# Kernel optimization log

Hardware: AMD Instinct MI355X
Metric: run time of the kernel (lower is better)

The kernel has to match this reference:

```python
import jax, jax.numpy as jnp
import numpy as np


def _gcn_conv(x, W, b, src, dst, num_nodes):
    # PyG GCNConv: h = x @ W; symmetric normalization with self-loops; scatter-add; + bias
    h = x @ W
    deg = jax.ops.segment_sum(jnp.ones_like(dst, dtype=h.dtype), dst, num_segments=num_nodes)
    dinv = jnp.where(deg > 0, jax.lax.rsqrt(deg), 0.0)
    norm = dinv[src] * dinv[dst]                         # [E]
    msgs = h[src] * norm[:, None]                        # [E, H] gather + scale
    out = jax.ops.segment_sum(msgs, dst, num_segments=num_nodes)
    return out + b


def setup_inputs() -> dict:
    key = jax.random.key(0)
    ks = jax.random.split(key, 10)
    N, E = 500000, 1000000
    IN, H, SIG = 3, 64, 24
    x = jax.random.uniform(ks[0], (N, IN), dtype=jnp.float32)
    edge_index = jax.random.randint(ks[1], (2, E), 0, N, dtype=jnp.int64)
    batch = jnp.zeros((N,), dtype=jnp.int64)
    def glorot(k, shape):
        lim = np.sqrt(6.0 / (shape[0] + shape[1]))
        return jax.random.uniform(k, shape, dtype=jnp.float32, minval=-lim, maxval=lim)
    return {
        "x": x,
        "edge_index": edge_index,
        "batch": batch,
        "W1": glorot(ks[2], (IN, H)), "b1": jnp.zeros((H,), jnp.float32),
        "W2": glorot(ks[3], (H, H)),  "b2": jnp.zeros((H,), jnp.float32),
        "W3": glorot(ks[4], (H, H)),  "b3": jnp.zeros((H,), jnp.float32),
        "Wfc": glorot(ks[5], (H, SIG)), "bfc": jnp.zeros((SIG,), jnp.float32),
    }


def reference(x, edge_index, batch, W1, b1, W2, b2, W3, b3, Wfc, bfc):
    N = x.shape[0]
    NUM_GRAPHS = 1  # batch is all zeros (single graph)
    # add self-loops once (GCNConv adds them per layer; identical edge set each layer)
    loop = jnp.arange(N, dtype=edge_index.dtype)
    src = jnp.concatenate([edge_index[0], loop])
    dst = jnp.concatenate([edge_index[1], loop])

    h = jax.nn.relu(_gcn_conv(x, W1, b1, src, dst, N))
    h = jax.nn.relu(_gcn_conv(h, W2, b2, src, dst, N))
    h = jax.nn.relu(_gcn_conv(h, W3, b3, src, dst, N))

    # global mean pool per graph
    sums = jax.ops.segment_sum(h, batch, num_segments=NUM_GRAPHS)          # [G, H]
    counts = jax.ops.segment_sum(jnp.ones((N,), h.dtype), batch, num_segments=NUM_GRAPHS)
    sig = sums / jnp.maximum(counts, 1.0)[:, None]

    return jnp.tanh(sig @ Wfc + bfc)  # [G, 24]
```

## Files before the change

### kernel.cpp

```cpp
#include <hip/hip_runtime.h>
#include <hip/hip_bf16.h>
#include <hip/hip_fp16.h>


#define ALIGN256(x) (((x) + 255) & ~(size_t)255)
#define NBUCK_MAX 512

typedef _Float16 half8 __attribute__((ext_vector_type(8)));
typedef _Float16 half4 __attribute__((ext_vector_type(4)));
typedef float f32x4 __attribute__((ext_vector_type(4)));
typedef int i32x4 __attribute__((ext_vector_type(4)));

__device__ __forceinline__ void dec16(i32x4 r, half8& a, half8& b) {
    i32x4 u, v;
    u.x = (int)(((unsigned)r.x << 8) & 0xFF00FF00u);
    u.y = (int)(((unsigned)r.x)      & 0xFF00FF00u);
    u.z = (int)(((unsigned)r.y << 8) & 0xFF00FF00u);
    u.w = (int)(((unsigned)r.y)      & 0xFF00FF00u);
    v.x = (int)(((unsigned)r.z << 8) & 0xFF00FF00u);
    v.y = (int)(((unsigned)r.z)      & 0xFF00FF00u);
    v.z = (int)(((unsigned)r.w << 8) & 0xFF00FF00u);
    v.w = (int)(((unsigned)r.w)      & 0xFF00FF00u);
    a = *(half8*)&u; b = *(half8*)&v;
}

__device__ __forceinline__ unsigned char enc8(float x) {
    unsigned short hb = __half_as_ushort(__float2half(x));
    return (unsigned char)((hb + 0x80u) >> 8);
}

__global__ __launch_bounds__(256) void hist_kernel(const int* __restrict__ ei, int E, int CE, int SH,
                                                   int* __restrict__ cnt_mat,
                                                   float* __restrict__ pool,
                                                   unsigned char* __restrict__ h8a,
                                                   unsigned char* __restrict__ h8b, int N) {
    __shared__ int h[NBUCK_MAX];
    const int t = threadIdx.x, blk = blockIdx.x;
    if (blk == 0) {
        if (t < 64) pool[t] = 0.f;
        if (t < 16) {
            ((int*)(h8a + (size_t)N * 64))[t] = 0;
            ((int*)(h8b + (size_t)N * 64))[t] = 0;
        }
    }
    for (int i = t; i < NBUCK_MAX; i += 256) h[i] = 0;
    __syncthreads();
    const int e0 = blk * CE, e1 = min(E, e0 + CE);
    for (int e = e0 + t; e < e1; e += 256)
        atomicAdd(&h[ei[E + e] >> SH], 1);
    __syncthreads();
    for (int i = t; i < NBUCK_MAX; i += 256) cnt_mat[blk * NBUCK_MAX + i] = h[i];
}

__global__ __launch_bounds__(64) void colscan_kernel(const int* __restrict__ cnt_mat,
                                                     int* __restrict__ base_mat,
                                                     int* __restrict__ tot, int nblk) {
    __shared__ int ls[64];
    const int j = blockIdx.x;
    const int t = threadIdx.x;
    const int PER = (nblk + 63) >> 6;
    const int b0 = t * PER, b1 = min(nblk, b0 + PER);
    int s = 0;
    for (int b = b0; b < b1; ++b) s += cnt_mat[b * NBUCK_MAX + j];
    ls[t] = s;
    __syncthreads();
    if (t == 0) {
        int run = 0;
        for (int k = 0; k < 64; ++k) { int v = ls[k]; ls[k] = run; run += v; }
        tot[j] = run;
    }
    __syncthreads();
    int run = ls[t];
    for (int b = b0; b < b1; ++b) {
        int v = cnt_mat[b * NBUCK_MAX + j];
        base_mat[b * NBUCK_MAX + j] = run;
        run += v;
    }
}

__global__ __launch_bounds__(256) void totscan_kernel(const int* __restrict__ tot,
                                                      int* __restrict__ startb, int NBK, int E) {
    __shared__ int ls[256];
    const int t = threadIdx.x;
    const int PER = (NBK + 255) >> 8;
    const int j0 = t * PER, j1 = min(NBK, j0 + PER);
    int s = 0;
    for (int j = j0; j < j1; ++j) s += tot[j];
    ls[t] = s;
    __syncthreads();
    if (t == 0) {
        int run = 0;
        for (int k = 0; k < 256; ++k) { int v = ls[k]; ls[k] = run; run += v; }
        startb[NBK] = E;
    }
    __syncthreads();
    int run = ls[t];
    for (int j = j0; j < j1; ++j) { startb[j] = run; run += tot[j]; }
}

__global__ __launch_bounds__(256) void scatter_kernel(const int* __restrict__ ei, int E, int CE, int SH,
                                                      const int* __restrict__ base_mat,
                                                      const int* __restrict__ start,
                                                      unsigned* __restrict__ bkt) {
    __shared__ int sbuf[4096];
    __shared__ unsigned short sb[4096];
    __shared__ int lh[NBUCK_MAX];
    __shared__ int lbase[NBUCK_MAX];
    __shared__ int cur[NBUCK_MAX];
    __shared__ int ls[256];
    const int t = threadIdx.x, blk = blockIdx.x;
    for (int i = t; i < NBUCK_MAX; i += 256) { lh[i] = 0; cur[i] = 0; }
    __syncthreads();
    const int e0 = blk * CE, e1 = min(E, e0 + CE);
    for (int e = e0 + t; e < e1; e += 256)
        atomicAdd(&lh[ei[E + e] >> SH], 1);
    __syncthreads();
    int a0 = lh[2 * t], a1 = lh[2 * t + 1];
    ls[t] = a0 + a1;
    __syncthreads();
    if (t == 0) {
        int run = 0;
        for (int k = 0; k < 256; ++k) { int v = ls[k]; ls[k] = run; run += v; }
    }
    __syncthreads();
    lbase[2 * t]     = ls[t];
    lbase[2 * t + 1] = ls[t] + a0;
    __syncthreads();
    const unsigned lowm = (1u << SH) - 1u;
    for (int e = e0 + t; e < e1; e += 256) {
        int s = ei[e], d = ei[E + e];
        int b = d >> SH;
        int r = atomicAdd(&cur[b], 1);
        int slot = lbase[b] + r;
        sbuf[slot] = (int)((((unsigned)d & lowm) << 21) | (unsigned)s);
        sb[slot] = (unsigned short)b;
    }
    __syncthreads();
    const int n = e1 - e0;
    for (int i = t; i < n; i += 256) {
        int b = sb[i];
        int dest = start[b] + base_mat[blk * NBUCK_MAX + b] + (i - lbase[b]);
        bkt[dest] = (unsigned)sbuf[i];
    }
}

__global__ __launch_bounds__(256) void build_kernel(const unsigned* __restrict__ bkt,
                                                    const int* __restrict__ start,
                                                    int SH, int nrows, int N,
                                                    const float* __restrict__ x,
                                                    int* __restrict__ ell, int* __restrict__ sec,
                                                    half4* __restrict__ xs) {
    __shared__ __align__(16) int loc[2048][8];
    const int t = threadIdx.x, j = blockIdx.x;
    const int R = 1 << SH;
    int4 z = make_int4(0, 0, 0, 0);
    for (int i = t; i < R * 2; i += 256) ((int4*)loc)[i] = z;
    __syncthreads();
    const int s0 = start[j], s1 = start[j + 1];
    for (int e = s0 + t; e < s1; e += 256) {
        unsigned p = bkt[e];
        int dl = (int)(p >> 21);
        int src = (int)(p & 0x1FFFFFu);
        int k = atomicAdd(&loc[dl][0], 1);
        if (k < 7) loc[dl][1 + k] = src;
        else if (k < 15) {
            int grow = (j << SH) + dl;
            sec[(size_t)grow * 8 + (k - 7)] = src;
        }
    }
    __syncthreads();
    const int base = j << SH;
    for (int i = t; i < R; i += 256) {
        int grow = base + i;
        if (grow < nrows) {
            int4* dst = (int4*)(ell + (size_t)grow * 8);
            dst[0] = ((int4*)&loc[i][0])[0];
            dst[1] = ((int4*)&loc[i][0])[1];
            if (grow < N) {
                float d = rsqrtf((float)(loc[i][0] + 1));
                half4 v;
                v[0] = (_Float16)(d * x[(size_t)grow * 3 + 0]);
                v[1] = (_Float16)(d * x[(size_t)grow * 3 + 1]);
                v[2] = (_Float16)(d * x[(size_t)grow * 3 + 2]);
                v[3] = (_Float16)0.f;
                xs[grow] = v;
            } else if (grow == N) {
                *(int2*)&xs[N] = make_int2(0, 0);
            }
        }
    }
}

__global__ __launch_bounds__(256) void layer1_kernel(const half4* __restrict__ xs,
                                                     const int* __restrict__ ell,
                                                     const int* __restrict__ sec,
                                                     const float* __restrict__ W1, const float* __restrict__ b1,
                                                     unsigned char* __restrict__ hout, int N) {
    __shared__ float4 a1S[256];
    const int t = threadIdx.x;
    const int jg = blockIdx.x * 256 + t;
    const bool valid = (jg < N);
    const int jc = valid ? jg : N;

    half4 sv = xs[jc];
    float sx = (float)sv[0], sy = (float)sv[1], sz = (float)sv[2];
    const int* row = ell + (size_t)(valid ? jg : 0) * 8;
    int4 e0 = *(const int4*)row;
    int4 e1 = *(const int4*)(row + 4);
    int craw = valid ? e0.x : 0;
    int deg = min(craw, 15);
    int i0 = (deg > 0) ? e0.y : N;
    int i1 = (deg > 1) ? e0.z : N;
    int i2 = (deg > 2) ? e0.w : N;
    int i3 = (deg > 3) ? e1.x : N;
    int i4 = (deg > 4) ? e1.y : N;
    int i5 = (deg > 5) ? e1.z : N;
    int i6 = (deg > 6) ? e1.w : N;
    half4 q0 = xs[i0], q1 = xs[i1], q2 = xs[i2], q3 = xs[i3];
    half4 q4 = xs[i4], q5 = xs[i5], q6 = xs[i6];
    sx += (float)q0[0] + (float)q1[0] + (float)q2[0] + (float)q3[0]
        + (float)q4[0] + (float)q5[0] + (float)q6[0];
    sy += (float)q0[1] + (float)q1[1] + (float)q2[1] + (float)q3[1]
        + (float)q4[1] + (float)q5[1] + (float)q6[1];
    sz += (float)q0[2] + (float)q1[2] + (float)q2[2] + (float)q3[2]
        + (float)q4[2] + (float)q5[2] + (float)q6[2];
    if (deg > 7) {
        const int* srow = sec + (size_t)jg * 8;
        for (int i = 7; i < deg; ++i) {
            half4 qq = xs[srow[i - 7]];
            sx += (float)qq[0]; sy += (float)qq[1]; sz += (float)qq[2];
        }
    }
    float dj = valid ? rsqrtf((float)(craw + 1)) : 0.f;
    a1S[t] = make_float4(dj * sx, dj * sy, dj * sz, dj);
    __syncthreads();

    const int l = t & 63, w = t >> 6;
    const float w0 = W1[l], w1 = W1[64 + l], w2 = W1[128 + l], bl = b1[l];
    const int base = blockIdx.x * 256 + w * 64;
    #pragma unroll 4
    for (int n = 0; n < 64; ++n) {
        int j2 = base + n;
        if (j2 >= N) break;
        float4 a = a1S[w * 64 + n];
        float v = fmaf(a.x, w0, fmaf(a.y, w1, fmaf(a.z, w2, bl)));
        hout[(size_t)j2 * 64 + l] = enc8(a.w * fmaxf(v, 0.f));
    }
}

template <int POOL>
__global__ __launch_bounds__(256) void layer_kernel(const unsigned char* __restrict__ hin,
                                                    const int* __restrict__ ell,
                                                    const int* __restrict__ sec,
                                                    const float* __restrict__ W, const float* __restrict__ bias,
                                                    unsigned char* __restrict__ hout, float* __restrict__ pool, int N) {
    const int t = threadIdx.x;
    const int l = t & 63;
    const int w = t >> 6;
    const int l15 = l & 15, q = l >> 4;
    const int m = l >> 2, qq = l & 3;
    const int cbase = l & ~3;

    __shared__ float red[256];
    __shared__ __align__(16) _Float16 wlds[8 * 64 * 8];
    __shared__ __align__(16) int tbuf[4][16 * 36];

    for (int c = t; c < 512; c += 256) {
        int f = c >> 6, ln = c & 63;
        int ct = f >> 1, kt = f & 1;
        int q2 = ln >> 4, m2 = ln & 15;
        half8 b;
        #pragma unroll
        for (int j = 0; j < 8; ++j) {
            int g = 4 * q2 + (j >> 1);
            int ii = g & 7, blk = g >> 3;
            int feat = 16 * blk + 4 * (ii >> 1) + (ii & 1) + 2 * (j & 1);
            b[j] = (_Float16)W[(kt * 32 + feat) * 64 + ct * 16 + m2];
        }
        *(half8*)&wlds[(size_t)c * 8] = b;
    }
    float bb[4];
    #pragma unroll
    for (int ct = 0; ct < 4; ++ct) bb[ct] = bias[ct * 16 + l15];
    __syncthreads();

    const char* hb = (const char*)hin;
    const int vlo = qq * 16;
    float ps0 = 0.f, ps1 = 0.f, ps2 = 0.f, ps3 = 0.f;

    const int ngroups = (N + 15) >> 4;
    const int gstride = gridDim.x * 4;
    for (int g = blockIdx.x * 4 + w; g < ngroups; g += gstride) {
        const int j0 = g << 4;
        const int jm = j0 + m;
        const bool validm = (jm < N);
        const int jsm = validm ? jm : N;

        i32x4 iv = *(const i32x4*)(ell + (size_t)jsm * 8 + (qq & 1) * 4);

        int cnt = __shfl(iv.x, cbase, 64);
        int s1  = __shfl(iv.y, cbase, 64);
        int s2  = __shfl(iv.z, cbase, 64);
        int s3  = __shfl(iv.w, cbase, 64);
        int s4  = __shfl(iv.x, cbase + 1, 64);
        int s5  = __shfl(iv.y, cbase + 1, 64);
        int s6  = __shfl(iv.z, cbase + 1, 64);
        int s7  = __shfl(iv.w, cbase + 1, 64);

        int craw = validm ? cnt : 0;
        int degc = min(craw, 15);
        float djv = rsqrtf((float)(craw + 1));

        int dmax = degc;
        dmax = max(dmax, __shfl_xor(dmax, 4, 64));
        dmax = max(dmax, __shfl_xor(dmax, 8, 64));
        dmax = max(dmax, __shfl_xor(dmax, 16, 64));
        dmax = max(dmax, __shfl_xor(dmax, 32, 64));

        s1 = (degc > 0) ? s1 : N;
        s2 = (degc > 1) ? s2 : N;
        s3 = (degc > 2) ? s3 : N;
        s4 = (degc > 3) ? s4 : N;
        s5 = (degc > 4) ? s5 : N;
        s6 = (degc > 5) ? s6 : N;
        s7 = (degc > 6) ? s7 : N;

        i32x4 rS = *(const i32x4*)(hb + ((size_t)jsm << 6) + vlo);
        i32x4 r1 = *(const i32x4*)(hb + ((size_t)(unsigned)s1 << 6) + vlo);
        i32x4 r2 = *(const i32x4*)(hb + ((size_t)(unsigned)s2 << 6) + vlo);
        i32x4 r3 = *(const i32x4*)(hb + ((size_t)(unsigned)s3 << 6) + vlo);
        i32x4 r4 = *(const i32x4*)(hb + ((size_t)(unsigned)s4 << 6) + vlo);
        const bool big = (dmax > 4);
        i32x4 r5, r6, r7;
        if (big) {
            r5 = *(const i32x4*)(hb + ((size_t)(unsigned)s5 << 6) + vlo);
            r6 = *(const i32x4*)(hb + ((size_t)(unsigned)s6 << 6) + vlo);
            r7 = *(const i32x4*)(hb + ((size_t)(unsigned)s7 << 6) + vlo);
        }

        half8 aA, aB, tA, tB;
        dec16(rS, aA, aB);
        dec16(r1, tA, tB); aA += tA; aB += tB;
        dec16(r2, tA, tB); aA += tA; aB += tB;
        dec16(r3, tA, tB); aA += tA; aB += tB;
        dec16(r4, tA, tB); aA += tA; aB += tB;
        if (big) {
            dec16(r5, tA, tB); aA += tA; aB += tB;
            dec16(r6, tA, tB); aA += tA; aB += tB;
            dec16(r7, tA, tB); aA += tA; aB += tB;
        }
        if (dmax > 7) {
            const int* srow = sec + (size_t)jsm * 8;
            #pragma unroll
            for (int ww = 8; ww < 16; ++ww) {
                int sr = (degc > ww - 1) ? srow[ww - 8] : N;
                i32x4 rt = *(const i32x4*)(hb + ((size_t)(unsigned)sr << 6) + vlo);
                dec16(rt, tA, tB); aA += tA; aB += tB;
            }
        }

        *(i32x4*)&tbuf[w][m * 36 + qq * 8]     = *(i32x4*)&aA;
        *(i32x4*)&tbuf[w][m * 36 + qq * 8 + 4] = *(i32x4*)&aB;
        half8 af0 = *(half8*)&tbuf[w][l15 * 36 + 4 * q];
        half8 af1 = *(half8*)&tbuf[w][l15 * 36 + 16 + 4 * q];

        const half8* wl = (const half8*)wlds;
        f32x4 c0 = {0.f, 0.f, 0.f, 0.f}, c1 = c0, c2 = c0, c3 = c0;
        c0 = __builtin_amdgcn_mfma_f32_16x16x32_f16(af0, wl[      l], c0, 0, 0, 0);
        c1 = __builtin_amdgcn_mfma_f32_16x16x32_f16(af0, wl[128 + l], c1, 0, 0, 0);
        c2 = __builtin_amdgcn_mfma_f32_16x16x32_f16(af0, wl[256 + l], c2, 0, 0, 0);
        c3 = __builtin_amdgcn_mfma_f32_16x16x32_f16(af0, wl[384 + l], c3, 0, 0, 0);
        c0 = __builtin_amdgcn_mfma_f32_16x16x32_f16(af1, wl[ 64 + l], c0, 0, 0, 0);
        c1 = __builtin_amdgcn_mfma_f32_16x16x32_f16(af1, wl[192 + l], c1, 0, 0, 0);
        c2 = __builtin_amdgcn_mfma_f32_16x16x32_f16(af1, wl[320 + l], c2, 0, 0, 0);
        c3 = __builtin_amdgcn_mfma_f32_16x16x32_f16(af1, wl[448 + l], c3, 0, 0, 0);

        if (POOL) {
            #pragma unroll
            for (int r = 0; r < 4; ++r) {
                int row = q * 4 + r;
                int gj = j0 + row;
                float djr = __shfl(djv, row << 2, 64);
                if (gj < N) {
                    ps0 += fmaxf(djr * c0[r] + bb[0], 0.f);
                    ps1 += fmaxf(djr * c1[r] + bb[1], 0.f);
                    ps2 += fmaxf(djr * c2[r] + bb[2], 0.f);
                    ps3 += fmaxf(djr * c3[r] + bb[3], 0.f);
                }
            }
        } else {
            #pragma unroll
            for (int r = 0; r < 4; ++r) {
                int row = q * 4 + r;
                int gj = j0 + row;
                float djr = __shfl(djv, row << 2, 64);
                if (gj < N) {
                    unsigned char* hp = hout + (size_t)gj * 64 + l15;
                    hp[0]  = enc8(djr * fmaxf(djr * c0[r] + bb[0], 0.f));
                    hp[16] = enc8(djr * fmaxf(djr * c1[r] + bb[1], 0.f));
                    hp[32] = enc8(djr * fmaxf(djr * c2[r] + bb[2], 0.f));
                    hp[48] = enc8(djr * fmaxf(djr * c3[r] + bb[3], 0.f));
                }
            }
        }
    }

    if (POOL) {
        ps0 += __shfl_xor(ps0, 16, 64); ps0 += __shfl_xor(ps0, 32, 64);
        ps1 += __shfl_xor(ps1, 16, 64); ps1 += __shfl_xor(ps1, 32, 64);
        ps2 += __shfl_xor(ps2, 16, 64); ps2 += __shfl_xor(ps2, 32, 64);
        ps3 += __shfl_xor(ps3, 16, 64); ps3 += __shfl_xor(ps3, 32, 64);
        if (q == 0) {
            red[w * 64 + l15]      = ps0;
            red[w * 64 + 16 + l15] = ps1;
            red[w * 64 + 32 + l15] = ps2;
            red[w * 64 + 48 + l15] = ps3;
        }
        __syncthreads();
        if (t < 64) {
            float s = red[t] + red[64 + t] + red[128 + t] + red[192 + t];
            atomicAdd(&pool[t], s);
        }
    }
}

__global__ __launch_bounds__(64) void final_kernel(const float* __restrict__ pool, const float* __restrict__ Wfc,
                                                   const float* __restrict__ bfc, float* __restrict__ out, int N) {
    int t = threadIdx.x;
    if (t < 24) {
        float inv = 1.0f / (float)N;
        float s = bfc[t];
        for (int c = 0; c < 64; ++c) s += pool[c] * inv * Wfc[c * 24 + t];
        out[t] = tanhf(s);
    }
}

extern "C" void kernel_launch(void* const* d_in, const int* in_sizes, int n_in,
                              void* d_out, int out_size, void* d_ws, size_t ws_size,
                              hipStream_t stream) {
    const float* x   = (const float*)d_in[0];
    const int*   ei  = (const int*)d_in[1];
    const float* W1  = (const float*)d_in[3];
    const float* b1  = (const float*)d_in[4];
    const float* W2  = (const float*)d_in[5];
    const float* b2  = (const float*)d_in[6];
    const float* W3  = (const float*)d_in[7];
    const float* b3  = (const float*)d_in[8];
    const float* Wfc = (const float*)d_in[9];
    const float* bfc = (const float*)d_in[10];
    float* out = (float*)d_out;

    const int N = in_sizes[2];
    const int E = in_sizes[1] / 2;

    size_t off = 0;
    auto take = [&](size_t bytes) -> char* {
        char* p = (char*)d_ws + off;
        off = ALIGN256(off + bytes);
        return p;
    };
    const int nrows = N + 16;
    int SH = 11;
    while ((((nrows - 1) >> SH) + 1) > NBUCK_MAX) ++SH;
    const int NBK = ((nrows - 1) >> SH) + 1;
    const int NCHUNK = (E + 4095) / 4096;
    const int CE = (E + NCHUNK - 1) / NCHUNK;

    int*           ell     = (int*)     take((size_t)nrows * 8 * 4);
    int*           sec     = (int*)     take((size_t)nrows * 8 * 4);
    unsigned*      bkt     = (unsigned*)take((size_t)E * 4);
    int*           cnt_mat = (int*)     take((size_t)NBUCK_MAX * NBUCK_MAX * 4);
    int*           base_mat= (int*)     take((size_t)NBUCK_MAX * NBUCK_MAX * 4);
    int*           tot     = (int*)     take(NBUCK_MAX * 4);
    int*           startb  = (int*)     take((NBUCK_MAX + 1) * 4);
    float*         pool    = (float*)   take(64 * 4);
    half4*         xs      = (half4*)   take(((size_t)N + 1) * 8);
    unsigned char* h8a     = (unsigned char*)take((size_t)(N + 1) * 64);
    unsigned char* h8b     = (unsigned char*)take((size_t)(N + 1) * 64);
    (void)ws_size; (void)n_in; (void)out_size;

    hist_kernel<<<NCHUNK, 256, 0, stream>>>(ei, E, CE, SH, cnt_mat, pool, h8a, h8b, N);
    colscan_kernel<<<NBK, 64, 0, stream>>>(cnt_mat, base_mat, tot, NCHUNK);
    totscan_kernel<<<1, 256, 0, stream>>>(tot, startb, NBK, E);
    scatter_kernel<<<NCHUNK, 256, 0, stream>>>(ei, E, CE, SH, base_mat, startb, bkt);
    build_kernel<<<NBK, 256, 0, stream>>>(bkt, startb, SH, nrows, N, x, ell, sec, xs);

    layer1_kernel<<<(N + 255) / 256, 256, 0, stream>>>(xs, ell, sec, W1, b1, h8a, N);

    int LB = 1024;
    const int ngroups = (N + 15) >> 4;
    const int maxb = (ngroups + 3) / 4;
    if (LB > maxb) LB = maxb;

    layer_kernel<0><<<LB, 256, 0, stream>>>(h8a, ell, sec, W2, b2, h8b, nullptr, N);

    layer_kernel<1><<<LB, 256, 0, stream>>>(h8b, ell, sec, W3, b3, nullptr, pool, N);

    final_kernel<<<1, 64, 0, stream>>>(pool, Wfc, bfc, out, N);
}
```

Measured before the change: 228.9 us.

## Fuse graph preprocessing kernels into one cooperative kernel with grid syncs

Replaces the five separate preprocessing launches (histogram, column scan, total scan, scatter, ELL build) with one cooperative kernel. The stages are separated by grid-wide syncs, and shared memory is reused through a union. The per-block histogram now stays in LDS for the scatter phase instead of being recomputed from the edge list. This is meant to remove inter-kernel launch gaps and the duplicate destination read. In exchange it adds grid-sync cost, needs all blocks co-resident under cooperative launch, and uses a larger LDS footprint per block, which may limit occupancy.

```diff
diff --git a/kernel.cpp b/kernel.cpp
--- a/kernel.cpp
+++ b/kernel.cpp
@@ -1,6 +1,9 @@
 #include <hip/hip_runtime.h>
 #include <hip/hip_bf16.h>
 #include <hip/hip_fp16.h>
+#include <hip/hip_cooperative_groups.h>
+
+namespace cg = cooperative_groups;
 
 
 #define ALIGN256(x) (((x) + 255) & ~(size_t)255)
@@ -29,13 +32,34 @@
     return (unsigned char)((hb + 0x80u) >> 8);
 }
 
-__global__ __launch_bounds__(256) void hist_kernel(const int* __restrict__ ei, int E, int CE, int SH,
-                                                   int* __restrict__ cnt_mat,
-                                                   float* __restrict__ pool,
-                                                   unsigned char* __restrict__ h8a,
-                                                   unsigned char* __restrict__ h8b, int N) {
-    __shared__ int h[NBUCK_MAX];
+__global__ __launch_bounds__(256) void chain_kernel(const int* __restrict__ ei, int E, int CE, int SH,
+                                                    int NBK, int NCHUNK, int nrows, int N,
+                                                    const float* __restrict__ x,
+                                                    int* __restrict__ cnt_mat, int* __restrict__ base_mat,
+                                                    int* __restrict__ tot, int* __restrict__ startb,
+                                                    unsigned* __restrict__ bkt,
+                                                    int* __restrict__ ell, int* __restrict__ sec,
+                                                    half4* __restrict__ xs,
+                                                    float* __restrict__ pool,
+                                                    unsigned char* __restrict__ h8a,
+                                                    unsigned char* __restrict__ h8b) {
     const int t = threadIdx.x, blk = blockIdx.x;
+    cg::grid_group grid = cg::this_grid();
+
+    __shared__ union U {
+        struct {
+            int lh[NBUCK_MAX];
+            int lbase[NBUCK_MAX];
+            int cur[NBUCK_MAX];
+            int ls[256];
+            int sbuf[4096];
+            unsigned short sb[4096];
+        } sc;
+        int slab[2048][8];
+    } u;
+
+    const int e0 = blk * CE, e1 = min(E, e0 + CE);
+
     if (blk == 0) {
         if (t < 64) pool[t] = 0.f;
         if (t < 16) {
@@ -43,149 +67,126 @@
             ((int*)(h8b + (size_t)N * 64))[t] = 0;
         }
     }
-    for (int i = t; i < NBUCK_MAX; i += 256) h[i] = 0;
+    for (int i = t; i < NBUCK_MAX; i += 256) { u.sc.lh[i] = 0; u.sc.cur[i] = 0; }
     __syncthreads();
-    const int e0 = blk * CE, e1 = min(E, e0 + CE);
-    for (int e = e0 + t; e < e1; e += 256)
-        atomicAdd(&h[ei[E + e] >> SH], 1);
+    if (blk < NCHUNK) {
+        for (int e = e0 + t; e < e1; e += 256)
+            atomicAdd(&u.sc.lh[ei[E + e] >> SH], 1);
+    }
     __syncthreads();
-    for (int i = t; i < NBUCK_MAX; i += 256) cnt_mat[blk * NBUCK_MAX + i] = h[i];
-}
-
-__global__ __launch_bounds__(64) void colscan_kernel(const int* __restrict__ cnt_mat,
-                                                     int* __restrict__ base_mat,
-                                                     int* __restrict__ tot, int nblk) {
-    __shared__ int ls[64];
-    const int j = blockIdx.x;
-    const int t = threadIdx.x;
-    const int PER = (nblk + 63) >> 6;
-    const int b0 = t * PER, b1 = min(nblk, b0 + PER);
-    int s = 0;
-    for (int b = b0; b < b1; ++b) s += cnt_mat[b * NBUCK_MAX + j];
-    ls[t] = s;
-    __syncthreads();
-    if (t == 0) {
-        int run = 0;
-        for (int k = 0; k < 64; ++k) { int v = ls[k]; ls[k] = run; run += v; }
-        tot[j] = run;
-    }
-    __syncthreads();
-    int run = ls[t];
-    for (int b = b0; b < b1; ++b) {
-        int v = cnt_mat[b * NBUCK_MAX + j];
-        base_mat[b * NBUCK_MAX + j] = run;
-        run += v;
-    }
-}
-
-__global__ __launch_bounds__(256) void totscan_kernel(const int* __restrict__ tot,
-                                                      int* __restrict__ startb, int NBK, int E) {
-    __shared__ int ls[256];
-    const int t = threadIdx.x;
-    const int PER = (NBK + 255) >> 8;
-    const int j0 = t * PER, j1 = min(NBK, j0 + PER);
-    int s = 0;
-    for (int j = j0; j < j1; ++j) s += tot[j];
-    ls[t] = s;
-    __syncthreads();
-    if (t == 0) {
-        int run = 0;
-        for (int k = 0; k < 256; ++k) { int v = ls[k]; ls[k] = run; run += v; }
-        startb[NBK] = E;
-    }
-    __syncthreads();
-    int run = ls[t];
-    for (int j = j0; j < j1; ++j) { startb[j] = run; run += tot[j]; }
-}
-
-__global__ __launch_bounds__(256) void scatter_kernel(const int* __restrict__ ei, int E, int CE, int SH,
-                                                      const int* __restrict__ base_mat,
-                                                      const int* __restrict__ start,
-                                                      unsigned* __restrict__ bkt) {
-    __shared__ int sbuf[4096];
-    __shared__ unsigned short sb[4096];
-    __shared__ int lh[NBUCK_MAX];
-    __shared__ int lbase[NBUCK_MAX];
-    __shared__ int cur[NBUCK_MAX];
-    __shared__ int ls[256];
-    const int t = threadIdx.x, blk = blockIdx.x;
-    for (int i = t; i < NBUCK_MAX; i += 256) { lh[i] = 0; cur[i] = 0; }
-    __syncthreads();
-    const int e0 = blk * CE, e1 = min(E, e0 + CE);
-    for (int e = e0 + t; e < e1; e += 256)
-        atomicAdd(&lh[ei[E + e] >> SH], 1);
-    __syncthreads();
-    int a0 = lh[2 * t], a1 = lh[2 * t + 1];
-    ls[t] = a0 + a1;
-    __syncthreads();
-    if (t == 0) {
-        int run = 0;
-        for (int k = 0; k < 256; ++k) { int v = ls[k]; ls[k] = run; run += v; }
-    }
-    __syncthreads();
-    lbase[2 * t]     = ls[t];
-    lbase[2 * t + 1] = ls[t] + a0;
-    __syncthreads();
-    const unsigned lowm = (1u << SH) - 1u;
-    for (int e = e0 + t; e < e1; e += 256) {
-        int s = ei[e], d = ei[E + e];
-        int b = d >> SH;
-        int r = atomicAdd(&cur[b], 1);
-        int slot = lbase[b] + r;
-        sbuf[slot] = (int)((((unsigned)d & lowm) << 21) | (unsigned)s);
-        sb[slot] = (unsigned short)b;
-    }
-    __syncthreads();
-    const int n = e1 - e0;
-    for (int i = t; i < n; i += 256) {
-        int b = sb[i];
-        int dest = start[b] + base_mat[blk * NBUCK_MAX + b] + (i - lbase[b]);
-        bkt[dest] = (unsigned)sbuf[i];
-    }
-}
-
-__global__ __launch_bounds__(256) void build_kernel(const unsigned* __restrict__ bkt,
-                                                    const int* __restrict__ start,
-                                                    int SH, int nrows, int N,
-                                                    const float* __restrict__ x,
-                                                    int* __restrict__ ell, int* __restrict__ sec,
-                                                    half4* __restrict__ xs) {
-    __shared__ __align__(16) int loc[2048][8];
-    const int t = threadIdx.x, j = blockIdx.x;
-    const int R = 1 << SH;
-    int4 z = make_int4(0, 0, 0, 0);
-    for (int i = t; i < R * 2; i += 256) ((int4*)loc)[i] = z;
-    __syncthreads();
-    const int s0 = start[j], s1 = start[j + 1];
-    for (int e = s0 + t; e < s1; e += 256) {
-        unsigned p = bkt[e];
-        int dl = (int)(p >> 21);
-        int src = (int)(p & 0x1FFFFFu);
-        int k = atomicAdd(&loc[dl][0], 1);
-        if (k < 7) loc[dl][1 + k] = src;
-        else if (k < 15) {
-            int grow = (j << SH) + dl;
-            sec[(size_t)grow * 8 + (k - 7)] = src;
-        }
-    }
-    __syncthreads();
-    const int base = j << SH;
-    for (int i = t; i < R; i += 256) {
-        int grow = base + i;
-        if (grow < nrows) {
-            int4* dst = (int4*)(ell + (size_t)grow * 8);
-            dst[0] = ((int4*)&loc[i][0])[0];
-            dst[1] = ((int4*)&loc[i][0])[1];
-            if (grow < N) {
-                float d = rsqrtf((float)(loc[i][0] + 1));
-                half4 v;
-                v[0] = (_Float16)(d * x[(size_t)grow * 3 + 0]);
-                v[1] = (_Float16)(d * x[(size_t)grow * 3 + 1]);
-                v[2] = (_Float16)(d * x[(size_t)grow * 3 + 2]);
-                v[3] = (_Float16)0.f;
-                xs[grow] = v;
-            } else if (grow == N) {
-                *(int2*)&xs[N] = make_int2(0, 0);
+    if (blk < NCHUNK)
+        for (int i = t; i < NBUCK_MAX; i += 256) cnt_mat[blk * NBUCK_MAX + i] = u.sc.lh[i];
+    grid.sync();
+
+    if (blk < NBK) {
+        const int j = blk;
+        const int PER = (NCHUNK + 255) >> 8;
+        const int b0 = t * PER, b1 = min(NCHUNK, b0 + PER);
+        int s = 0;
+        for (int b = b0; b < b1; ++b) s += cnt_mat[b * NBUCK_MAX + j];
+        u.sc.ls[t] = s;
+        __syncthreads();
+        if (t == 0) {
+            int run = 0;
+            for (int k = 0; k < 256; ++k) { int v = u.sc.ls[k]; u.sc.ls[k] = run; run += v; }
+            tot[j] = run;
+        }
+        __syncthreads();
+        int run = u.sc.ls[t];
+        for (int b = b0; b < b1; ++b) {
+            int v = cnt_mat[b * NBUCK_MAX + j];
+            base_mat[b * NBUCK_MAX + j] = run;
+            run += v;
+        }
+    }
+    grid.sync();
+
+    if (blk == 0) {
+        const int PER = (NBK + 255) >> 8;
+        const int j0 = t * PER, j1 = min(NBK, j0 + PER);
+        int s = 0;
+        for (int j = j0; j < j1; ++j) s += tot[j];
+        u.sc.ls[t] = s;
+        __syncthreads();
+        if (t == 0) {
+            int run = 0;
+            for (int k = 0; k < 256; ++k) { int v = u.sc.ls[k]; u.sc.ls[k] = run; run += v; }
+            startb[NBK] = E;
+        }
+        __syncthreads();
+        int run = u.sc.ls[t];
+        for (int j = j0; j < j1; ++j) { startb[j] = run; run += tot[j]; }
+    }
+    grid.sync();
+
+    if (blk < NCHUNK) {
+        int a0 = u.sc.lh[2 * t], a1 = u.sc.lh[2 * t + 1];
+        u.sc.ls[t] = a0 + a1;
+        __syncthreads();
+        if (t == 0) {
+            int run = 0;
+            for (int k = 0; k < 256; ++k) { int v = u.sc.ls[k]; u.sc.ls[k] = run; run += v; }
+        }
+        __syncthreads();
+        u.sc.lbase[2 * t]     = u.sc.ls[t];
+        u.sc.lbase[2 * t + 1] = u.sc.ls[t] + a0;
+        __syncthreads();
+        const unsigned lowm = (1u << SH) - 1u;
+        for (int e = e0 + t; e < e1; e += 256) {
+            int s = ei[e], d = ei[E + e];
+            int b = d >> SH;
+            int r = atomicAdd(&u.sc.cur[b], 1);
+            int slot = u.sc.lbase[b] + r;
+            u.sc.sbuf[slot] = (int)((((unsigned)d & lowm) << 21) | (unsigned)s);
+            u.sc.sb[slot] = (unsigned short)b;
+        }
+        __syncthreads();
+        const int n = e1 - e0;
+        for (int i = t; i < n; i += 256) {
+            int b = u.sc.sb[i];
+            int dest = startb[b] + base_mat[blk * NBUCK_MAX + b] + (i - u.sc.lbase[b]);
+            bkt[dest] = (unsigned)u.sc.sbuf[i];
+        }
+    }
+    grid.sync();
+
+    if (blk < NBK) {
+        const int j = blk;
+        const int R = 1 << SH;
+        int4 z = make_int4(0, 0, 0, 0);
+        for (int i = t; i < R * 2; i += 256) ((int4*)u.slab)[i] = z;
+        __syncthreads();
+        const int s0 = startb[j], s1 = startb[j + 1];
+        for (int e = s0 + t; e < s1; e += 256) {
+            unsigned p = bkt[e];
+            int dl = (int)(p >> 21);
+            int src = (int)(p & 0x1FFFFFu);
+            int k = atomicAdd(&u.slab[dl][0], 1);
+            if (k < 7) u.slab[dl][1 + k] = src;
+            else if (k < 15) {
+                int grow = (j << SH) + dl;
+                sec[(size_t)grow * 8 + (k - 7)] = src;
+            }
+        }
+        __syncthreads();
+        const int base = j << SH;
+        for (int i = t; i < R; i += 256) {
+            int grow = base + i;
+            if (grow < nrows) {
+                int4* dst = (int4*)(ell + (size_t)grow * 8);
+                dst[0] = ((int4*)&u.slab[i][0])[0];
+                dst[1] = ((int4*)&u.slab[i][0])[1];
+                if (grow < N) {
+                    float d = rsqrtf((float)(u.slab[i][0] + 1));
+                    half4 v;
+                    v[0] = (_Float16)(d * x[(size_t)grow * 3 + 0]);
+                    v[1] = (_Float16)(d * x[(size_t)grow * 3 + 1]);
+                    v[2] = (_Float16)(d * x[(size_t)grow * 3 + 2]);
+                    v[3] = (_Float16)0.f;
+                    xs[grow] = v;
+                } else if (grow == N) {
+                    *(int2*)&xs[N] = make_int2(0, 0);
+                }
             }
         }
     }
@@ -479,11 +480,19 @@
     unsigned char* h8b     = (unsigned char*)take((size_t)(N + 1) * 64);
     (void)ws_size; (void)n_in; (void)out_size;
 
-    hist_kernel<<<NCHUNK, 256, 0, stream>>>(ei, E, CE, SH, cnt_mat, pool, h8a, h8b, N);
-    colscan_kernel<<<NBK, 64, 0, stream>>>(cnt_mat, base_mat, tot, NCHUNK);
-    totscan_kernel<<<1, 256, 0, stream>>>(tot, startb, NBK, E);
-    scatter_kernel<<<NCHUNK, 256, 0, stream>>>(ei, E, CE, SH, base_mat, startb, bkt);
-    build_kernel<<<NBK, 256, 0, stream>>>(bkt, startb, SH, nrows, N, x, ell, sec, xs);
+    {
+        int grid_n = (NCHUNK > NBK) ? NCHUNK : NBK;
+        const int* ei_a = ei; int E_a = E, CE_a = CE, SH_a = SH, NBK_a = NBK,
+                   NCHUNK_a = NCHUNK, nrows_a = nrows, N_a = N;
+        const float* x_a = x;
+        void* args[] = { (void*)&ei_a, (void*)&E_a, (void*)&CE_a, (void*)&SH_a,
+                         (void*)&NBK_a, (void*)&NCHUNK_a, (void*)&nrows_a, (void*)&N_a,
+                         (void*)&x_a, (void*)&cnt_mat, (void*)&base_mat, (void*)&tot,
+                         (void*)&startb, (void*)&bkt, (void*)&ell, (void*)&sec,
+                         (void*)&xs, (void*)&pool, (void*)&h8a, (void*)&h8b };
+        hipLaunchCooperativeKernel((void*)chain_kernel, dim3(grid_n), dim3(256),
+                                   args, 0, stream);
+    }
 
     layer1_kernel<<<(N + 255) / 256, 256, 0, stream>>>(xs, ell, sec, W1, b1, h8a, N);
 
```

New measurement: 348.6 us. +52.2%, slower.
